# Kernel optimization log

Measured on AMD Instinct MI355X. Metric: run time of the kernel, lower is better.

The kernel has to match this reference:

```python
import jax, jax.numpy as jnp
import numpy as np

HEADS = 16
D_MODEL = 1024
GROUP = 4
SEQ = 2048
HEAD_DIM = D_MODEL // HEADS          # 64
KV_HEADS = HEADS // GROUP            # 4


def rope_tables(head_dim, seq_len, base=10000.0):
    # NOTE: faithful to source: exp = -2*arange(0,d,2)/d  (steps of 2 -> base^{-4j/d})
    exp = -2.0 * jnp.arange(0, head_dim, 2, dtype=jnp.float32) / head_dim
    thetas = jnp.power(base, exp)                       # [d/2]
    m = jnp.arange(seq_len, dtype=jnp.float32)          # [S]
    freq = jnp.outer(m, thetas)                         # [S, d/2]
    return jnp.cos(freq), jnp.sin(freq)


def apply_rope(x, cos, sin):
    # x: [B,S,H,D]; complex rotation on consecutive pairs
    B, S, H, D = x.shape
    xr = x.reshape(B, S, H, D // 2, 2)
    x0, x1 = xr[..., 0], xr[..., 1]
    c = cos[None, :S, None, :]
    s = sin[None, :S, None, :]
    out = jnp.stack([x0 * c - x1 * s, x0 * s + x1 * c], axis=-1)
    return out.reshape(B, S, H, D)


def setup_inputs() -> dict:
    key = jax.random.key(0)
    ks = jax.random.split(key, 8)
    B = 1
    q = jax.random.normal(ks[0], (B, SEQ, D_MODEL), dtype=jnp.float32)
    k = jax.random.normal(ks[1], (B, SEQ, D_MODEL), dtype=jnp.float32)
    v = jax.random.normal(ks[2], (B, SEQ, D_MODEL), dtype=jnp.float32)
    mask = jnp.tril(jnp.ones((SEQ, SEQ), dtype=jnp.int32))[None]  # causal [B,S,S]
    sc = 0.02
    Wq = jax.random.normal(ks[3], (D_MODEL, D_MODEL), dtype=jnp.float32) * sc
    Wk = jax.random.normal(ks[4], (D_MODEL, D_MODEL // GROUP), dtype=jnp.float32) * sc
    Wv = jax.random.normal(ks[5], (D_MODEL, D_MODEL // GROUP), dtype=jnp.float32) * sc
    Wo = jax.random.normal(ks[6], (D_MODEL, D_MODEL), dtype=jnp.float32) * sc
    bq = jnp.zeros((D_MODEL,), jnp.float32)
    bk = jnp.zeros((D_MODEL // GROUP,), jnp.float32)
    bv = jnp.zeros((D_MODEL // GROUP,), jnp.float32)
    bo = jnp.zeros((D_MODEL,), jnp.float32)
    return {"q": q, "k": k, "v": v, "mask": mask, "Wq": Wq, "bq": bq,
            "Wk": Wk, "bk": bk, "Wv": Wv, "bv": bv, "Wo": Wo, "bo": bo}


def reference(q, k, v, mask, Wq, bq, Wk, bk, Wv, bv, Wo, bo):
    B, S, _ = q.shape
    cos, sin = rope_tables(HEAD_DIM, S)
    qh = (q @ Wq + bq).reshape(B, S, HEADS, HEAD_DIM)
    kh = (k @ Wk + bk).reshape(B, S, KV_HEADS, HEAD_DIM)
    vh = (v @ Wv + bv).reshape(B, S, KV_HEADS, HEAD_DIM)
    qh = apply_rope(qh, cos, sin)
    kh = apply_rope(kh, cos, sin)
    qh = qh.transpose(0, 2, 1, 3)                       # [B,H,S,D]
    kh = kh.transpose(0, 2, 1, 3)                       # [B,Hkv,S,D]
    vh = vh.transpose(0, 2, 1, 3)
    # torch .repeat tiles: query head j attends kv head j % KV_HEADS
    kh = jnp.tile(kh, (1, GROUP, 1, 1))                 # [B,H,S,D]
    vh = jnp.tile(vh, (1, GROUP, 1, 1))
    scores = jnp.einsum('bhqd,bhkd->bhqk', qh, kh) / jnp.sqrt(
        jnp.asarray(HEAD_DIM, dtype=qh.dtype))
    scores = jnp.where(mask[:, None, :, :] == 0, -jnp.inf, scores)
    attn = jax.nn.softmax(scores, axis=-1)
    out = jnp.einsum('bhqk,bhkd->bhqd', attn, vh)
    out = out.transpose(0, 2, 1, 3).reshape(B, S, D_MODEL)
    return out @ Wo + bo
```

## Files before the change

kernel.cpp:

```cpp
#include <hip/hip_runtime.h>
#include <hip/hip_bf16.h>
#include <math.h>


#define SEQ 2048
#define DM 1024
#define HD 64

using u16 = unsigned short;
typedef __attribute__((ext_vector_type(8))) short bf16x8;
typedef __attribute__((ext_vector_type(4))) float f32x4;

#define QSCALE 0.18033688011112042f

__device__ __forceinline__ u16 f2b(float f) {
    union { float f; unsigned int i; } v; v.f = f;
    unsigned int u = v.i;
    return (u16)((u + 0x7fffu + ((u >> 16) & 1u)) >> 16);
}
__device__ __forceinline__ u16 f2b_fast(float f) {
    union { float f; unsigned int i; } v; v.f = f;
    return (u16)((v.i + 0x8000u) >> 16);
}

__global__ __launch_bounds__(256) void prep_kernel(
    const float* __restrict__ qin, const float* __restrict__ kin, const float* __restrict__ vin,
    const float* __restrict__ Wq, const float* __restrict__ Wk,
    const float* __restrict__ Wv, const float* __restrict__ Wo,
    u16* __restrict__ Xq, u16* __restrict__ Xk, u16* __restrict__ Xv,
    u16* __restrict__ Wt, u16* __restrict__ wot, float2* __restrict__ rope)
{
    const int b = blockIdx.x;
    const int t = threadIdx.x;

    if (b < 640) {
        __shared__ short T[64][72];
        const float* W; u16* dst; int N, t0, rowoff;
        if (b < 256)      { W = Wq; dst = Wt;  N = 1024; t0 = b;       rowoff = 0; }
        else if (b < 320) { W = Wk; dst = Wt;  N = 256;  t0 = b - 256; rowoff = 1024; }
        else if (b < 384) { W = Wv; dst = Wt;  N = 256;  t0 = b - 320; rowoff = 1280; }
        else              { W = Wo; dst = wot; N = 1024; t0 = b - 384; rowoff = 0; }
        const int ntn = N >> 6;
        const int k0 = (t0 / ntn) * 64, n0 = (t0 % ntn) * 64;
        const int r = t >> 4, c4 = (t & 15) * 4;
        #pragma unroll
        for (int rr = 0; rr < 4; ++rr) {
            const int k = r + rr * 16;
            float4 w4 = *reinterpret_cast<const float4*>(W + (size_t)(k0 + k) * N + n0 + c4);
            T[c4 + 0][k] = (short)f2b(w4.x);
            T[c4 + 1][k] = (short)f2b(w4.y);
            T[c4 + 2][k] = (short)f2b(w4.z);
            T[c4 + 3][k] = (short)f2b(w4.w);
        }
        __syncthreads();
        const int n = t >> 2, ck = (t & 3) * 16;
        u16* dp = dst + (size_t)(rowoff + n0 + n) * DM + k0 + ck;
        *reinterpret_cast<bf16x8*>(dp)     = *reinterpret_cast<const bf16x8*>(&T[n][ck]);
        *reinterpret_cast<bf16x8*>(dp + 8) = *reinterpret_cast<const bf16x8*>(&T[n][ck + 8]);
    } else if (b < 1408) {
        const int idx = b - 640;
        const int which = idx >> 8;
        const int ib = idx & 255;
        const float* src = (which == 0) ? qin : (which == 1) ? kin : vin;
        u16* dst = (which == 0) ? Xq : (which == 1) ? Xk : Xv;
        const size_t base = (size_t)ib * 8192 + (size_t)t * 32;
        #pragma unroll
        for (int c = 0; c < 4; ++c) {
            float4 x0 = *reinterpret_cast<const float4*>(src + base + c * 8);
            float4 x1 = *reinterpret_cast<const float4*>(src + base + c * 8 + 4);
            bf16x8 o;
            o[0] = (short)f2b(x0.x); o[1] = (short)f2b(x0.y);
            o[2] = (short)f2b(x0.z); o[3] = (short)f2b(x0.w);
            o[4] = (short)f2b(x1.x); o[5] = (short)f2b(x1.y);
            o[6] = (short)f2b(x1.z); o[7] = (short)f2b(x1.w);
            *reinterpret_cast<bf16x8*>(dst + base + c * 8) = o;
        }
    } else {
        const int m = (b - 1408) * 256 + t;
        float2* rp = rope + (size_t)m * 32;
        for (int pi = 0; pi < 32; ++pi) {
            const float theta = exp2f(-0.8304820237f * (float)pi);
            float sn, cs;
            sincosf((float)m * theta, &sn, &cs);
            rp[pi] = make_float2(cs, sn);
        }
    }
}

__global__ __launch_bounds__(256) void proj_mfma(
    const u16* __restrict__ Xq, const u16* __restrict__ Xk, const u16* __restrict__ Xv,
    const u16* __restrict__ Wt,
    const float* __restrict__ bq, const float* __restrict__ bk, const float* __restrict__ bv,
    const float2* __restrict__ rope,
    u16* __restrict__ Qr, u16* __restrict__ Kr, u16* __restrict__ Vrt)
{
    const int n0 = blockIdx.x * 64, m0 = blockIdx.y * 64;
    const int zone = (n0 < 1024) ? 0 : (n0 < 1280) ? 1 : 2;
    const u16* __restrict__ Az = (zone == 0) ? Xq : (zone == 1) ? Xk : Xv;

    __shared__ short As[2][64][72];
    __shared__ short Bs[2][64][72];

    const int t = threadIdx.x;
    const int w = t >> 6, lane = t & 63, lm = lane & 15, quad = lane >> 4;
    const int sr = t >> 2, sc = (t & 3) * 16;

    f32x4 acc[4] = { {0,0,0,0}, {0,0,0,0}, {0,0,0,0}, {0,0,0,0} };

    const u16* ap_ = Az + (size_t)(m0 + sr) * DM + sc;
    const u16* bp_ = Wt + (size_t)(n0 + sr) * DM + sc;
    bf16x8 aR0 = *reinterpret_cast<const bf16x8*>(ap_);
    bf16x8 aR1 = *reinterpret_cast<const bf16x8*>(ap_ + 8);
    bf16x8 bR0 = *reinterpret_cast<const bf16x8*>(bp_);
    bf16x8 bR1 = *reinterpret_cast<const bf16x8*>(bp_ + 8);

    for (int k0 = 0; k0 < DM; k0 += 64) {
        const int buf = (k0 >> 6) & 1;
        *reinterpret_cast<bf16x8*>(&As[buf][sr][sc])     = aR0;
        *reinterpret_cast<bf16x8*>(&As[buf][sr][sc + 8]) = aR1;
        *reinterpret_cast<bf16x8*>(&Bs[buf][sr][sc])     = bR0;
        *reinterpret_cast<bf16x8*>(&Bs[buf][sr][sc + 8]) = bR1;
        if (k0 + 64 < DM) {
            aR0 = *reinterpret_cast<const bf16x8*>(ap_ + k0 + 64);
            aR1 = *reinterpret_cast<const bf16x8*>(ap_ + k0 + 72);
            bR0 = *reinterpret_cast<const bf16x8*>(bp_ + k0 + 64);
            bR1 = *reinterpret_cast<const bf16x8*>(bp_ + k0 + 72);
        }
        __syncthreads();
        bf16x8 af0 = *reinterpret_cast<const bf16x8*>(&As[buf][16 * w + lm][quad * 8]);
        bf16x8 af1 = *reinterpret_cast<const bf16x8*>(&As[buf][16 * w + lm][32 + quad * 8]);
        #pragma unroll
        for (int nb = 0; nb < 4; ++nb) {
            bf16x8 b0 = *reinterpret_cast<const bf16x8*>(&Bs[buf][16 * nb + lm][quad * 8]);
            bf16x8 b1 = *reinterpret_cast<const bf16x8*>(&Bs[buf][16 * nb + lm][32 + quad * 8]);
            acc[nb] = __builtin_amdgcn_mfma_f32_16x16x32_bf16(af0, b0, acc[nb], 0, 0, 0);
            acc[nb] = __builtin_amdgcn_mfma_f32_16x16x32_bf16(af1, b1, acc[nb], 0, 0, 0);
        }
        __syncthreads();
    }

    const float* __restrict__ bias = (zone == 0) ? bq : (zone == 1) ? bk : bv;
    const int nbase = (zone == 0) ? n0 : (zone == 1) ? (n0 - 1024) : (n0 - 1280);
    const int head = nbase >> 6;
    #pragma unroll
    for (int nb = 0; nb < 4; ++nb) {
        const int d = 16 * nb + lm;
        const float bvv = bias[nbase + d];
        float vals[4];
        #pragma unroll
        for (int r = 0; r < 4; ++r) vals[r] = acc[nb][r] + bvv;
        if (zone != 2) {
            const int pi = d >> 1;
            const bool odd = (lm & 1);
            const float sca = (zone == 0) ? QSCALE : 1.0f;
            u16* op = (zone == 0 ? Qr : Kr) + (size_t)head * SEQ * HD;
            #pragma unroll
            for (int r = 0; r < 4; ++r) {
                const int m = m0 + 16 * w + quad * 4 + r;
                const float2 cs2 = rope[(size_t)m * 32 + pi];
                float x  = vals[r];
                float xp = __shfl_xor(x, 1);
                float o  = (odd ? (xp * cs2.y + x * cs2.x)
                                : (x * cs2.x - xp * cs2.y)) * sca;
                op[(size_t)m * HD + d] = f2b(o);
            }
        } else {
            u16* vp = Vrt + ((size_t)head * HD + d) * SEQ;
            #pragma unroll
            for (int r = 0; r < 4; ++r) {
                const int m = m0 + 16 * w + quad * 4 + r;
                const int within = m & 63;
                const int pos = (m & ~63) + 4 * (within & 15) + (within >> 4);
                vp[pos] = f2b(vals[r]);
            }
        }
    }
}

__global__ __launch_bounds__(512) void attn_mfma(
    const u16* __restrict__ Qr, const u16* __restrict__ Kr, const u16* __restrict__ Vrt,
    u16* __restrict__ AO)
{
    const int h  = blockIdx.x;
    const int qy = blockIdx.y;
    const int kvh = h & 3;

    __shared__ u16 Ks[2][64][72];
    __shared__ u16 Vt[2][64][72];
    __shared__ u16 Ps[8][16][76];

    const int t = threadIdx.x;
    const int w = t >> 6, lane = t & 63, lm = lane & 15, quad = lane >> 4;
    const int team = w >> 2, wt = w & 3;
    const int qt  = team ? (31 - qy) : qy;
    const int qtb = 31 - qy;

    {
        const int row = lane >> 2, c = (lane & 3) * 16;
        const u16* qp = Qr + ((size_t)h * SEQ + qt * 64 + wt * 16 + row) * HD + c;
        *reinterpret_cast<bf16x8*>(&Ps[w][row][c])     = *reinterpret_cast<const bf16x8*>(qp);
        *reinterpret_cast<bf16x8*>(&Ps[w][row][c + 8]) = *reinterpret_cast<const bf16x8*>(qp + 8);
    }
    const bf16x8 aq0 = *reinterpret_cast<const bf16x8*>(&Ps[w][lm][quad * 8]);
    const bf16x8 aq1 = *reinterpret_cast<const bf16x8*>(&Ps[w][lm][32 + quad * 8]);

    f32x4 O[4] = { {0,0,0,0}, {0,0,0,0}, {0,0,0,0}, {0,0,0,0} };
    float lp[4] = { 0.f, 0.f, 0.f, 0.f };

    const int srow = t >> 3, sc2 = (t & 7) * 8;
    const u16* kb_ = Kr  + ((size_t)kvh * SEQ + srow) * HD + sc2;
    const u16* vb_ = Vrt + ((size_t)kvh * HD + srow) * SEQ + sc2;
    bf16x8 kR = *reinterpret_cast<const bf16x8*>(kb_);
    bf16x8 vR = *reinterpret_cast<const bf16x8*>(vb_);

    for (int kt = 0; kt <= qtb; ++kt) {
        const int buf = kt & 1;
        *reinterpret_cast<bf16x8*>(&Ks[buf][srow][sc2]) = kR;
        *reinterpret_cast<bf16x8*>(&Vt[buf][srow][sc2]) = vR;
        if (kt < qtb) {
            kR = *reinterpret_cast<const bf16x8*>(kb_ + (size_t)(kt + 1) * 64 * HD);
            vR = *reinterpret_cast<const bf16x8*>(vb_ + (size_t)(kt + 1) * 64);
        }
        __syncthreads();

        if (kt <= qt) {
            f32x4 s[4];
            #pragma unroll
            for (int nb = 0; nb < 4; ++nb) {
                bf16x8 b0 = *reinterpret_cast<const bf16x8*>(&Ks[buf][16 * nb + lm][quad * 8]);
                bf16x8 b1 = *reinterpret_cast<const bf16x8*>(&Ks[buf][16 * nb + lm][32 + quad * 8]);
                f32x4 zz = { 0.f, 0.f, 0.f, 0.f };
                zz = __builtin_amdgcn_mfma_f32_16x16x32_bf16(aq0, b0, zz, 0, 0, 0);
                s[nb] = __builtin_amdgcn_mfma_f32_16x16x32_bf16(aq1, b1, zz, 0, 0, 0);
            }

            if (kt == qt) {
                #pragma unroll
                for (int nb = 0; nb < 4; ++nb)
                    #pragma unroll
                    for (int r = 0; r < 4; ++r)
                        if (16 * nb + lm > 16 * wt + quad * 4 + r) s[nb][r] = -INFINITY;
            }

            #pragma unroll
            for (int r = 0; r < 4; ++r) {
                u16 pk[4];
                #pragma unroll
                for (int nb = 0; nb < 4; ++nb) {
                    float e = __builtin_amdgcn_exp2f(fminf(s[nb][r], 126.f));
                    lp[r] += e;
                    pk[nb] = f2b_fast(e);
                }
                *reinterpret_cast<uint2*>(&Ps[w][quad * 4 + r][4 * lm]) =
                    *reinterpret_cast<uint2*>(pk);
            }

            const bf16x8 ap0 = *reinterpret_cast<const bf16x8*>(&Ps[w][lm][quad * 8]);
            const bf16x8 ap1 = *reinterpret_cast<const bf16x8*>(&Ps[w][lm][32 + quad * 8]);
            #pragma unroll
            for (int db = 0; db < 4; ++db) {
                bf16x8 v0 = *reinterpret_cast<const bf16x8*>(&Vt[buf][16 * db + lm][quad * 8]);
                bf16x8 v1 = *reinterpret_cast<const bf16x8*>(&Vt[buf][16 * db + lm][32 + quad * 8]);
                O[db] = __builtin_amdgcn_mfma_f32_16x16x32_bf16(ap0, v0, O[db], 0, 0, 0);
                O[db] = __builtin_amdgcn_mfma_f32_16x16x32_bf16(ap1, v1, O[db], 0, 0, 0);
            }
        }
    }

    #pragma unroll
    for (int r = 0; r < 4; ++r) {
        #pragma unroll
        for (int off = 1; off < 16; off <<= 1)
            lp[r] += __shfl_xor(lp[r], off);
        const float inv = 1.0f / lp[r];
        const size_t row = (size_t)(qt * 64 + 16 * wt + quad * 4 + r) * DM + (size_t)h * HD;
        #pragma unroll
        for (int db = 0; db < 4; ++db)
            AO[row + 16 * db + lm] = f2b(O[db][r] * inv);
    }
}

__global__ __launch_bounds__(256) void oproj_mfma(
    const u16* __restrict__ AO, const u16* __restrict__ wot,
    const float* __restrict__ bo, float* __restrict__ out)
{
    __shared__ short As[2][64][72];
    __shared__ short Bs[2][64][72];
    const int t = threadIdx.x;
    const int w = t >> 6, lane = t & 63, lm = lane & 15, quad = lane >> 4;
    const int m0 = blockIdx.y * 64, n0 = blockIdx.x * 64;
    const int sr = t >> 2, sc = (t & 3) * 16;

    f32x4 acc[4] = { {0,0,0,0}, {0,0,0,0}, {0,0,0,0}, {0,0,0,0} };

    const u16* ap_ = AO  + (size_t)(m0 + sr) * DM + sc;
    const u16* bp_ = wot + (size_t)(n0 + sr) * DM + sc;
    bf16x8 aR0 = *reinterpret_cast<const bf16x8*>(ap_);
    bf16x8 aR1 = *reinterpret_cast<const bf16x8*>(ap_ + 8);
    bf16x8 bR0 = *reinterpret_cast<const bf16x8*>(bp_);
    bf16x8 bR1 = *reinterpret_cast<const bf16x8*>(bp_ + 8);

    for (int k0 = 0; k0 < DM; k0 += 64) {
        const int buf = (k0 >> 6) & 1;
        *reinterpret_cast<bf16x8*>(&As[buf][sr][sc])     = aR0;
        *reinterpret_cast<bf16x8*>(&As[buf][sr][sc + 8]) = aR1;
        *reinterpret_cast<bf16x8*>(&Bs[buf][sr][sc])     = bR0;
        *reinterpret_cast<bf16x8*>(&Bs[buf][sr][sc + 8]) = bR1;
        if (k0 + 64 < DM) {
            aR0 = *reinterpret_cast<const bf16x8*>(ap_ + k0 + 64);
            aR1 = *reinterpret_cast<const bf16x8*>(ap_ + k0 + 72);
            bR0 = *reinterpret_cast<const bf16x8*>(bp_ + k0 + 64);
            bR1 = *reinterpret_cast<const bf16x8*>(bp_ + k0 + 72);
        }
        __syncthreads();
        bf16x8 af0 = *reinterpret_cast<const bf16x8*>(&As[buf][16 * w + lm][quad * 8]);
        bf16x8 af1 = *reinterpret_cast<const bf16x8*>(&As[buf][16 * w + lm][32 + quad * 8]);
        #pragma unroll
        for (int nb = 0; nb < 4; ++nb) {
            bf16x8 b0 = *reinterpret_cast<const bf16x8*>(&Bs[buf][16 * nb + lm][quad * 8]);
            bf16x8 b1 = *reinterpret_cast<const bf16x8*>(&Bs[buf][16 * nb + lm][32 + quad * 8]);
            acc[nb] = __builtin_amdgcn_mfma_f32_16x16x32_bf16(af0, b0, acc[nb], 0, 0, 0);
            acc[nb] = __builtin_amdgcn_mfma_f32_16x16x32_bf16(af1, b1, acc[nb], 0, 0, 0);
        }
        __syncthreads();
    }

    #pragma unroll
    for (int nb = 0; nb < 4; ++nb) {
        const int dl = 16 * nb + lm;
        const float bv = bo[n0 + dl];
        #pragma unroll
        for (int r = 0; r < 4; ++r) {
            const int m = m0 + 16 * w + quad * 4 + r;
            out[(size_t)m * DM + n0 + dl] = acc[nb][r] + bv;
        }
    }
}

extern "C" void kernel_launch(void* const* d_in, const int* in_sizes, int n_in,
                              void* d_out, int out_size, void* d_ws, size_t ws_size,
                              hipStream_t stream)
{
    const float* q  = (const float*)d_in[0];
    const float* k  = (const float*)d_in[1];
    const float* v  = (const float*)d_in[2];
    const float* Wq = (const float*)d_in[4];
    const float* bq = (const float*)d_in[5];
    const float* Wk = (const float*)d_in[6];
    const float* bk = (const float*)d_in[7];
    const float* Wv = (const float*)d_in[8];
    const float* bv = (const float*)d_in[9];
    const float* Wo = (const float*)d_in[10];
    const float* bo = (const float*)d_in[11];
    float* out = (float*)d_out;

    u16* Xq  = (u16*)d_ws;
    u16* Xk  = Xq  + (size_t)SEQ * DM;
    u16* Xv  = Xk  + (size_t)SEQ * DM;
    u16* Wt  = Xv  + (size_t)SEQ * DM;
    u16* wot = Wt  + (size_t)1536 * 1024;
    u16* Qr  = wot + (size_t)1024 * 1024;
    u16* Kr  = Qr  + (size_t)16 * SEQ * HD;
    u16* Vrt = Kr  + (size_t)4 * SEQ * HD;
    u16* AO  = Vrt + (size_t)4 * SEQ * HD;
    float2* rope = (float2*)(AO + (size_t)SEQ * DM);

    hipLaunchKernelGGL(prep_kernel, dim3(1416), dim3(256), 0, stream,
                       q, k, v, Wq, Wk, Wv, Wo, Xq, Xk, Xv, Wt, wot, rope);
    hipLaunchKernelGGL(proj_mfma, dim3(24, 32), dim3(256), 0, stream,
                       Xq, Xk, Xv, Wt, bq, bk, bv, rope, Qr, Kr, Vrt);
    hipLaunchKernelGGL(attn_mfma, dim3(16, 16), dim3(512), 0, stream,
                       Qr, Kr, Vrt, AO);
    hipLaunchKernelGGL(oproj_mfma, dim3(16, 32), dim3(256), 0, stream,
                       AO, wot, bo, out);
}
```

Baseline: 167.6 us.

## Give each attention wave 32 query rows to reuse K/V fragments across two MFMA tiles

The attention kernel drops from 512 to 256 threads per block, and each wave now handles 32 query rows (two 16-row MFMA tiles) instead of 16. Each K and V fragment read from LDS feeds two MFMAs, which halves LDS reads per unit of compute and the per-thread share of the K/V staging cost. In exchange, register use per wave roughly doubles (accumulators, scores, Q fragments) and there are half as many waves per block. That may lower occupancy and latency hiding in a grid of only 256 blocks.

After: 180.7 us. 1.08x slower.

```diff
diff --git a/kernel.cpp b/kernel.cpp
--- a/kernel.cpp
+++ b/kernel.cpp
@@ -177,7 +177,7 @@
     }
 }
 
-__global__ __launch_bounds__(512) void attn_mfma(
+__global__ __launch_bounds__(256) void attn_mfma(
     const u16* __restrict__ Qr, const u16* __restrict__ Kr, const u16* __restrict__ Vrt,
     u16* __restrict__ AO)
 {
@@ -187,97 +187,128 @@
 
     __shared__ u16 Ks[2][64][72];
     __shared__ u16 Vt[2][64][72];
-    __shared__ u16 Ps[8][16][76];
+    __shared__ u16 Ps[4][32][76];
 
     const int t = threadIdx.x;
     const int w = t >> 6, lane = t & 63, lm = lane & 15, quad = lane >> 4;
-    const int team = w >> 2, wt = w & 3;
+    const int team = w >> 1, tw = w & 1;
     const int qt  = team ? (31 - qy) : qy;
     const int qtb = 31 - qy;
 
     {
-        const int row = lane >> 2, c = (lane & 3) * 16;
-        const u16* qp = Qr + ((size_t)h * SEQ + qt * 64 + wt * 16 + row) * HD + c;
-        *reinterpret_cast<bf16x8*>(&Ps[w][row][c])     = *reinterpret_cast<const bf16x8*>(qp);
-        *reinterpret_cast<bf16x8*>(&Ps[w][row][c + 8]) = *reinterpret_cast<const bf16x8*>(qp + 8);
-    }
-    const bf16x8 aq0 = *reinterpret_cast<const bf16x8*>(&Ps[w][lm][quad * 8]);
-    const bf16x8 aq1 = *reinterpret_cast<const bf16x8*>(&Ps[w][lm][32 + quad * 8]);
-
-    f32x4 O[4] = { {0,0,0,0}, {0,0,0,0}, {0,0,0,0}, {0,0,0,0} };
-    float lp[4] = { 0.f, 0.f, 0.f, 0.f };
-
-    const int srow = t >> 3, sc2 = (t & 7) * 8;
+        const int row = lane & 31, cb = (lane >> 5) * 32;
+        const u16* qp = Qr + ((size_t)h * SEQ + qt * 64 + tw * 32 + row) * HD + cb;
+        #pragma unroll
+        for (int i = 0; i < 4; ++i)
+            *reinterpret_cast<bf16x8*>(&Ps[w][row][cb + 8 * i]) =
+                *reinterpret_cast<const bf16x8*>(qp + 8 * i);
+    }
+    bf16x8 aq[2][2];
+    #pragma unroll
+    for (int qb = 0; qb < 2; ++qb) {
+        aq[qb][0] = *reinterpret_cast<const bf16x8*>(&Ps[w][16 * qb + lm][quad * 8]);
+        aq[qb][1] = *reinterpret_cast<const bf16x8*>(&Ps[w][16 * qb + lm][32 + quad * 8]);
+    }
+
+    f32x4 O[2][4] = { { {0,0,0,0}, {0,0,0,0}, {0,0,0,0}, {0,0,0,0} },
+                      { {0,0,0,0}, {0,0,0,0}, {0,0,0,0}, {0,0,0,0} } };
+    float lp[2][4] = { {0.f,0.f,0.f,0.f}, {0.f,0.f,0.f,0.f} };
+
+    const int srow = t >> 2, sc2 = (t & 3) * 16;
     const u16* kb_ = Kr  + ((size_t)kvh * SEQ + srow) * HD + sc2;
     const u16* vb_ = Vrt + ((size_t)kvh * HD + srow) * SEQ + sc2;
-    bf16x8 kR = *reinterpret_cast<const bf16x8*>(kb_);
-    bf16x8 vR = *reinterpret_cast<const bf16x8*>(vb_);
+    bf16x8 kR0 = *reinterpret_cast<const bf16x8*>(kb_);
+    bf16x8 kR1 = *reinterpret_cast<const bf16x8*>(kb_ + 8);
+    bf16x8 vR0 = *reinterpret_cast<const bf16x8*>(vb_);
+    bf16x8 vR1 = *reinterpret_cast<const bf16x8*>(vb_ + 8);
 
     for (int kt = 0; kt <= qtb; ++kt) {
         const int buf = kt & 1;
-        *reinterpret_cast<bf16x8*>(&Ks[buf][srow][sc2]) = kR;
-        *reinterpret_cast<bf16x8*>(&Vt[buf][srow][sc2]) = vR;
+        *reinterpret_cast<bf16x8*>(&Ks[buf][srow][sc2])     = kR0;
+        *reinterpret_cast<bf16x8*>(&Ks[buf][srow][sc2 + 8]) = kR1;
+        *reinterpret_cast<bf16x8*>(&Vt[buf][srow][sc2])     = vR0;
+        *reinterpret_cast<bf16x8*>(&Vt[buf][srow][sc2 + 8]) = vR1;
         if (kt < qtb) {
-            kR = *reinterpret_cast<const bf16x8*>(kb_ + (size_t)(kt + 1) * 64 * HD);
-            vR = *reinterpret_cast<const bf16x8*>(vb_ + (size_t)(kt + 1) * 64);
+            kR0 = *reinterpret_cast<const bf16x8*>(kb_ + (size_t)(kt + 1) * 64 * HD);
+            kR1 = *reinterpret_cast<const bf16x8*>(kb_ + (size_t)(kt + 1) * 64 * HD + 8);
+            vR0 = *reinterpret_cast<const bf16x8*>(vb_ + (size_t)(kt + 1) * 64);
+            vR1 = *reinterpret_cast<const bf16x8*>(vb_ + (size_t)(kt + 1) * 64 + 8);
         }
         __syncthreads();
 
         if (kt <= qt) {
-            f32x4 s[4];
+            f32x4 s[2][4];
             #pragma unroll
             for (int nb = 0; nb < 4; ++nb) {
                 bf16x8 b0 = *reinterpret_cast<const bf16x8*>(&Ks[buf][16 * nb + lm][quad * 8]);
                 bf16x8 b1 = *reinterpret_cast<const bf16x8*>(&Ks[buf][16 * nb + lm][32 + quad * 8]);
-                f32x4 zz = { 0.f, 0.f, 0.f, 0.f };
-                zz = __builtin_amdgcn_mfma_f32_16x16x32_bf16(aq0, b0, zz, 0, 0, 0);
-                s[nb] = __builtin_amdgcn_mfma_f32_16x16x32_bf16(aq1, b1, zz, 0, 0, 0);
+                #pragma unroll
+                for (int qb = 0; qb < 2; ++qb) {
+                    f32x4 zz = { 0.f, 0.f, 0.f, 0.f };
+                    zz = __builtin_amdgcn_mfma_f32_16x16x32_bf16(aq[qb][0], b0, zz, 0, 0, 0);
+                    s[qb][nb] = __builtin_amdgcn_mfma_f32_16x16x32_bf16(aq[qb][1], b1, zz, 0, 0, 0);
+                }
             }
 
             if (kt == qt) {
                 #pragma unroll
-                for (int nb = 0; nb < 4; ++nb)
+                for (int qb = 0; qb < 2; ++qb)
                     #pragma unroll
-                    for (int r = 0; r < 4; ++r)
-                        if (16 * nb + lm > 16 * wt + quad * 4 + r) s[nb][r] = -INFINITY;
-            }
-
-            #pragma unroll
-            for (int r = 0; r < 4; ++r) {
-                u16 pk[4];
+                    for (int nb = 0; nb < 4; ++nb)
+                        #pragma unroll
+                        for (int r = 0; r < 4; ++r)
+                            if (16 * nb + lm > 32 * tw + 16 * qb + quad * 4 + r)
+                                s[qb][nb][r] = -INFINITY;
+            }
+
+            #pragma unroll
+            for (int qb = 0; qb < 2; ++qb)
                 #pragma unroll
-                for (int nb = 0; nb < 4; ++nb) {
-                    float e = __builtin_amdgcn_exp2f(fminf(s[nb][r], 126.f));
-                    lp[r] += e;
-                    pk[nb] = f2b_fast(e);
+                for (int r = 0; r < 4; ++r) {
+                    u16 pk[4];
+                    #pragma unroll
+                    for (int nb = 0; nb < 4; ++nb) {
+                        float e = __builtin_amdgcn_exp2f(fminf(s[qb][nb][r], 126.f));
+                        lp[qb][r] += e;
+                        pk[nb] = f2b_fast(e);
+                    }
+                    *reinterpret_cast<uint2*>(&Ps[w][16 * qb + quad * 4 + r][4 * lm]) =
+                        *reinterpret_cast<uint2*>(pk);
                 }
-                *reinterpret_cast<uint2*>(&Ps[w][quad * 4 + r][4 * lm]) =
-                    *reinterpret_cast<uint2*>(pk);
-            }
-
-            const bf16x8 ap0 = *reinterpret_cast<const bf16x8*>(&Ps[w][lm][quad * 8]);
-            const bf16x8 ap1 = *reinterpret_cast<const bf16x8*>(&Ps[w][lm][32 + quad * 8]);
+
+            bf16x8 ap[2][2];
+            #pragma unroll
+            for (int qb = 0; qb < 2; ++qb) {
+                ap[qb][0] = *reinterpret_cast<const bf16x8*>(&Ps[w][16 * qb + lm][quad * 8]);
+                ap[qb][1] = *reinterpret_cast<const bf16x8*>(&Ps[w][16 * qb + lm][32 + quad * 8]);
+            }
             #pragma unroll
             for (int db = 0; db < 4; ++db) {
                 bf16x8 v0 = *reinterpret_cast<const bf16x8*>(&Vt[buf][16 * db + lm][quad * 8]);
                 bf16x8 v1 = *reinterpret_cast<const bf16x8*>(&Vt[buf][16 * db + lm][32 + quad * 8]);
-                O[db] = __builtin_amdgcn_mfma_f32_16x16x32_bf16(ap0, v0, O[db], 0, 0, 0);
-                O[db] = __builtin_amdgcn_mfma_f32_16x16x32_bf16(ap1, v1, O[db], 0, 0, 0);
+                #pragma unroll
+                for (int qb = 0; qb < 2; ++qb) {
+                    O[qb][db] = __builtin_amdgcn_mfma_f32_16x16x32_bf16(ap[qb][0], v0, O[qb][db], 0, 0, 0);
+                    O[qb][db] = __builtin_amdgcn_mfma_f32_16x16x32_bf16(ap[qb][1], v1, O[qb][db], 0, 0, 0);
+                }
             }
         }
     }
 
     #pragma unroll
-    for (int r = 0; r < 4; ++r) {
-        #pragma unroll
-        for (int off = 1; off < 16; off <<= 1)
-            lp[r] += __shfl_xor(lp[r], off);
-        const float inv = 1.0f / lp[r];
-        const size_t row = (size_t)(qt * 64 + 16 * wt + quad * 4 + r) * DM + (size_t)h * HD;
-        #pragma unroll
-        for (int db = 0; db < 4; ++db)
-            AO[row + 16 * db + lm] = f2b(O[db][r] * inv);
-    }
+    for (int qb = 0; qb < 2; ++qb)
+        #pragma unroll
+        for (int r = 0; r < 4; ++r) {
+            #pragma unroll
+            for (int off = 1; off < 16; off <<= 1)
+                lp[qb][r] += __shfl_xor(lp[qb][r], off);
+            const float inv = 1.0f / lp[qb][r];
+            const size_t row = (size_t)(qt * 64 + 32 * tw + 16 * qb + quad * 4 + r) * DM
+                             + (size_t)h * HD;
+            #pragma unroll
+            for (int db = 0; db < 4; ++db)
+                AO[row + 16 * db + lm] = f2b(O[qb][db][r] * inv);
+        }
 }
 
 __global__ __launch_bounds__(256) void oproj_mfma(
@@ -369,7 +400,7 @@
                        q, k, v, Wq, Wk, Wv, Wo, Xq, Xk, Xv, Wt, wot, rope);
     hipLaunchKernelGGL(proj_mfma, dim3(24, 32), dim3(256), 0, stream,
                        Xq, Xk, Xv, Wt, bq, bk, bv, rope, Qr, Kr, Vrt);
-    hipLaunchKernelGGL(attn_mfma, dim3(16, 16), dim3(512), 0, stream,
+    hipLaunchKernelGGL(attn_mfma, dim3(16, 16), dim3(256), 0, stream,
                        Qr, Kr, Vrt, AO);
     hipLaunchKernelGGL(oproj_mfma, dim3(16, 32), dim3(256), 0, stream,
                        AO, wot, bo, out);
```

## Split paired-tile attention blocks into independent 256-thread blocks per query tile

Applied to the files above, without the earlier changes.

The attention kernel previously paired a short and a long causal query tile in one 512-thread block sharing K/V loads, with the short team idling after its diagonal. Each block now handles one query tile with 4 waves, and the 1D grid of 512 blocks is ordered so short tiles come first and long tiles later. Each block loads only the K/V tiles it needs, which removes the idle waves and lets the scheduler pack blocks more freely. The cost is that K/V tiles are no longer shared between paired tiles, so global and LDS traffic goes up, and the long-tile blocks at the end of the grid may leave a tail of imbalance.

Result: no change. 166.0 us (-0.9%).

```diff
diff --git a/kernel.cpp b/kernel.cpp
--- a/kernel.cpp
+++ b/kernel.cpp
@@ -177,27 +177,25 @@
     }
 }
 
-__global__ __launch_bounds__(512) void attn_mfma(
+__global__ __launch_bounds__(256) void attn_mfma(
     const u16* __restrict__ Qr, const u16* __restrict__ Kr, const u16* __restrict__ Vrt,
     u16* __restrict__ AO)
 {
-    const int h  = blockIdx.x;
-    const int qy = blockIdx.y;
+    const int bid = blockIdx.x;
+    const int h  = bid & 15;
+    const int qt = (bid < 256) ? (bid >> 4) : 31 - ((bid - 256) >> 4);
     const int kvh = h & 3;
 
     __shared__ u16 Ks[2][64][72];
     __shared__ u16 Vt[2][64][72];
-    __shared__ u16 Ps[8][16][76];
+    __shared__ u16 Ps[4][16][76];
 
     const int t = threadIdx.x;
     const int w = t >> 6, lane = t & 63, lm = lane & 15, quad = lane >> 4;
-    const int team = w >> 2, wt = w & 3;
-    const int qt  = team ? (31 - qy) : qy;
-    const int qtb = 31 - qy;
 
     {
         const int row = lane >> 2, c = (lane & 3) * 16;
-        const u16* qp = Qr + ((size_t)h * SEQ + qt * 64 + wt * 16 + row) * HD + c;
+        const u16* qp = Qr + ((size_t)h * SEQ + qt * 64 + w * 16 + row) * HD + c;
         *reinterpret_cast<bf16x8*>(&Ps[w][row][c])     = *reinterpret_cast<const bf16x8*>(qp);
         *reinterpret_cast<bf16x8*>(&Ps[w][row][c + 8]) = *reinterpret_cast<const bf16x8*>(qp + 8);
     }
@@ -207,63 +205,67 @@
     f32x4 O[4] = { {0,0,0,0}, {0,0,0,0}, {0,0,0,0}, {0,0,0,0} };
     float lp[4] = { 0.f, 0.f, 0.f, 0.f };
 
-    const int srow = t >> 3, sc2 = (t & 7) * 8;
+    const int srow = t >> 2, sc2 = (t & 3) * 16;
     const u16* kb_ = Kr  + ((size_t)kvh * SEQ + srow) * HD + sc2;
     const u16* vb_ = Vrt + ((size_t)kvh * HD + srow) * SEQ + sc2;
-    bf16x8 kR = *reinterpret_cast<const bf16x8*>(kb_);
-    bf16x8 vR = *reinterpret_cast<const bf16x8*>(vb_);
-
-    for (int kt = 0; kt <= qtb; ++kt) {
+    bf16x8 kR0 = *reinterpret_cast<const bf16x8*>(kb_);
+    bf16x8 kR1 = *reinterpret_cast<const bf16x8*>(kb_ + 8);
+    bf16x8 vR0 = *reinterpret_cast<const bf16x8*>(vb_);
+    bf16x8 vR1 = *reinterpret_cast<const bf16x8*>(vb_ + 8);
+
+    for (int kt = 0; kt <= qt; ++kt) {
         const int buf = kt & 1;
-        *reinterpret_cast<bf16x8*>(&Ks[buf][srow][sc2]) = kR;
-        *reinterpret_cast<bf16x8*>(&Vt[buf][srow][sc2]) = vR;
-        if (kt < qtb) {
-            kR = *reinterpret_cast<const bf16x8*>(kb_ + (size_t)(kt + 1) * 64 * HD);
-            vR = *reinterpret_cast<const bf16x8*>(vb_ + (size_t)(kt + 1) * 64);
-        }
-        __syncthreads();
-
-        if (kt <= qt) {
-            f32x4 s[4];
+        *reinterpret_cast<bf16x8*>(&Ks[buf][srow][sc2])     = kR0;
+        *reinterpret_cast<bf16x8*>(&Ks[buf][srow][sc2 + 8]) = kR1;
+        *reinterpret_cast<bf16x8*>(&Vt[buf][srow][sc2])     = vR0;
+        *reinterpret_cast<bf16x8*>(&Vt[buf][srow][sc2 + 8]) = vR1;
+        if (kt < qt) {
+            kR0 = *reinterpret_cast<const bf16x8*>(kb_ + (size_t)(kt + 1) * 64 * HD);
+            kR1 = *reinterpret_cast<const bf16x8*>(kb_ + (size_t)(kt + 1) * 64 * HD + 8);
+            vR0 = *reinterpret_cast<const bf16x8*>(vb_ + (size_t)(kt + 1) * 64);
+            vR1 = *reinterpret_cast<const bf16x8*>(vb_ + (size_t)(kt + 1) * 64 + 8);
+        }
+        __syncthreads();
+
+        f32x4 s[4];
+        #pragma unroll
+        for (int nb = 0; nb < 4; ++nb) {
+            bf16x8 b0 = *reinterpret_cast<const bf16x8*>(&Ks[buf][16 * nb + lm][quad * 8]);
+            bf16x8 b1 = *reinterpret_cast<const bf16x8*>(&Ks[buf][16 * nb + lm][32 + quad * 8]);
+            f32x4 zz = { 0.f, 0.f, 0.f, 0.f };
+            zz = __builtin_amdgcn_mfma_f32_16x16x32_bf16(aq0, b0, zz, 0, 0, 0);
+            s[nb] = __builtin_amdgcn_mfma_f32_16x16x32_bf16(aq1, b1, zz, 0, 0, 0);
+        }
+
+        if (kt == qt) {
+            #pragma unroll
+            for (int nb = 0; nb < 4; ++nb)
+                #pragma unroll
+                for (int r = 0; r < 4; ++r)
+                    if (16 * nb + lm > 16 * w + quad * 4 + r) s[nb][r] = -INFINITY;
+        }
+
+        #pragma unroll
+        for (int r = 0; r < 4; ++r) {
+            u16 pk[4];
             #pragma unroll
             for (int nb = 0; nb < 4; ++nb) {
-                bf16x8 b0 = *reinterpret_cast<const bf16x8*>(&Ks[buf][16 * nb + lm][quad * 8]);
-                bf16x8 b1 = *reinterpret_cast<const bf16x8*>(&Ks[buf][16 * nb + lm][32 + quad * 8]);
-                f32x4 zz = { 0.f, 0.f, 0.f, 0.f };
-                zz = __builtin_amdgcn_mfma_f32_16x16x32_bf16(aq0, b0, zz, 0, 0, 0);
-                s[nb] = __builtin_amdgcn_mfma_f32_16x16x32_bf16(aq1, b1, zz, 0, 0, 0);
+                float e = __builtin_amdgcn_exp2f(fminf(s[nb][r], 126.f));
+                lp[r] += e;
+                pk[nb] = f2b_fast(e);
             }
-
-            if (kt == qt) {
-                #pragma unroll
-                for (int nb = 0; nb < 4; ++nb)
-                    #pragma unroll
-                    for (int r = 0; r < 4; ++r)
-                        if (16 * nb + lm > 16 * wt + quad * 4 + r) s[nb][r] = -INFINITY;
-            }
-
-            #pragma unroll
-            for (int r = 0; r < 4; ++r) {
-                u16 pk[4];
-                #pragma unroll
-                for (int nb = 0; nb < 4; ++nb) {
-                    float e = __builtin_amdgcn_exp2f(fminf(s[nb][r], 126.f));
-                    lp[r] += e;
-                    pk[nb] = f2b_fast(e);
-                }
-                *reinterpret_cast<uint2*>(&Ps[w][quad * 4 + r][4 * lm]) =
-                    *reinterpret_cast<uint2*>(pk);
-            }
-
-            const bf16x8 ap0 = *reinterpret_cast<const bf16x8*>(&Ps[w][lm][quad * 8]);
-            const bf16x8 ap1 = *reinterpret_cast<const bf16x8*>(&Ps[w][lm][32 + quad * 8]);
-            #pragma unroll
-            for (int db = 0; db < 4; ++db) {
-                bf16x8 v0 = *reinterpret_cast<const bf16x8*>(&Vt[buf][16 * db + lm][quad * 8]);
-                bf16x8 v1 = *reinterpret_cast<const bf16x8*>(&Vt[buf][16 * db + lm][32 + quad * 8]);
-                O[db] = __builtin_amdgcn_mfma_f32_16x16x32_bf16(ap0, v0, O[db], 0, 0, 0);
-                O[db] = __builtin_amdgcn_mfma_f32_16x16x32_bf16(ap1, v1, O[db], 0, 0, 0);
-            }
+            *reinterpret_cast<uint2*>(&Ps[w][quad * 4 + r][4 * lm]) =
+                *reinterpret_cast<uint2*>(pk);
+        }
+
+        const bf16x8 ap0 = *reinterpret_cast<const bf16x8*>(&Ps[w][lm][quad * 8]);
+        const bf16x8 ap1 = *reinterpret_cast<const bf16x8*>(&Ps[w][lm][32 + quad * 8]);
+        #pragma unroll
+        for (int db = 0; db < 4; ++db) {
+            bf16x8 v0 = *reinterpret_cast<const bf16x8*>(&Vt[buf][16 * db + lm][quad * 8]);
+            bf16x8 v1 = *reinterpret_cast<const bf16x8*>(&Vt[buf][16 * db + lm][32 + quad * 8]);
+            O[db] = __builtin_amdgcn_mfma_f32_16x16x32_bf16(ap0, v0, O[db], 0, 0, 0);
+            O[db] = __builtin_amdgcn_mfma_f32_16x16x32_bf16(ap1, v1, O[db], 0, 0, 0);
         }
     }
 
@@ -273,7 +275,7 @@
         for (int off = 1; off < 16; off <<= 1)
             lp[r] += __shfl_xor(lp[r], off);
         const float inv = 1.0f / lp[r];
-        const size_t row = (size_t)(qt * 64 + 16 * wt + quad * 4 + r) * DM + (size_t)h * HD;
+        const size_t row = (size_t)(qt * 64 + 16 * w + quad * 4 + r) * DM + (size_t)h * HD;
         #pragma unroll
         for (int db = 0; db < 4; ++db)
             AO[row + 16 * db + lm] = f2b(O[db][r] * inv);
@@ -369,7 +371,7 @@
                        q, k, v, Wq, Wk, Wv, Wo, Xq, Xk, Xv, Wt, wot, rope);
     hipLaunchKernelGGL(proj_mfma, dim3(24, 32), dim3(256), 0, stream,
                        Xq, Xk, Xv, Wt, bq, bk, bv, rope, Qr, Kr, Vrt);
-    hipLaunchKernelGGL(attn_mfma, dim3(16, 16), dim3(512), 0, stream,
+    hipLaunchKernelGGL(attn_mfma, dim3(512), dim3(256), 0, stream,
                        Qr, Kr, Vrt, AO);
     hipLaunchKernelGGL(oproj_mfma, dim3(16, 32), dim3(256), 0, stream,
                        AO, wot, bo, out);
```
